# Kernel tuning notes

Hardware: AMD Instinct MI355X
Metric: run time of the kernel (lower is better)

The kernel has to match this reference:

```python
import jax, jax.numpy as jnp
import numpy as np

V = 50257   # vocab size (output_size / num_words)
H = 500     # hidden_size
S = 256     # source sequence length
MAXLEN = 64 # greedy decode steps
SOS = 1


def _gru_scan(xs, Wih, Whh, bih, bhh, reverse=False):
    """Run a GRU over xs: (S, Din) -> (outputs (S,H), final hidden (H,)).
    PyTorch gate order: r, z, n."""
    gx = xs @ Wih.T + bih  # (S, 3H), input-side gates precomputed
    Hh = Whh.shape[1]
    h0 = jnp.zeros((Hh,), dtype=xs.dtype)

    def step(h, g):
        gh = Whh @ h + bhh
        rx, zx, nx = jnp.split(g, 3)
        rh, zh, nh = jnp.split(gh, 3)
        r = jax.nn.sigmoid(rx + rh)
        z = jax.nn.sigmoid(zx + zh)
        n = jnp.tanh(nx + r * nh)
        h2 = (1.0 - z) * n + z * h
        return h2, h2

    hT, ys = jax.lax.scan(step, h0, gx, reverse=reverse)
    return ys, hT


def _gru_cell(x, h, Wih, Whh, bih, bhh):
    gx = Wih @ x + bih
    gh = Whh @ h + bhh
    rx, zx, nx = jnp.split(gx, 3)
    rh, zh, nh = jnp.split(gh, 3)
    r = jax.nn.sigmoid(rx + rh)
    z = jax.nn.sigmoid(zx + zh)
    n = jnp.tanh(nx + r * nh)
    return (1.0 - z) * n + z * h


def setup_inputs() -> dict:
    key = jax.random.key(0)
    ks = jax.random.split(key, 32)

    def p(k, shape):
        return jax.random.normal(k, shape, dtype=jnp.float32) * 0.05

    inp = {}
    inp["input_seq"] = jax.random.randint(ks[0], (S, 1), 0, V)
    inp["input_length"] = S
    inp["max_length"] = MAXLEN
    inp["emb"] = p(ks[1], (V, H))
    i = 2
    for name, din in [("enc0f", H), ("enc0b", H), ("enc1f", 2 * H), ("enc1b", 2 * H)]:
        inp[name + "_Wih"] = p(ks[i], (3 * H, din)); i += 1
        inp[name + "_Whh"] = p(ks[i], (3 * H, H)); i += 1
        inp[name + "_bih"] = p(ks[i], (3 * H,)); i += 1
        inp[name + "_bhh"] = p(ks[i], (3 * H,)); i += 1
    inp["dec_Wih"] = p(ks[i], (2, 3 * H, H)); i += 1
    inp["dec_Whh"] = p(ks[i], (2, 3 * H, H)); i += 1
    inp["dec_bih"] = p(ks[i], (2, 3 * H)); i += 1
    inp["dec_bhh"] = p(ks[i], (2, 3 * H)); i += 1
    inp["concat_W"] = p(ks[i], (H, 2 * H)); i += 1
    inp["concat_b"] = p(ks[i], (H,)); i += 1
    inp["out_W"] = p(ks[i], (V, H)); i += 1
    inp["out_b"] = p(ks[i], (V,)); i += 1
    return inp


def reference(input_seq, input_length, max_length, emb,
              enc0f_Wih, enc0f_Whh, enc0f_bih, enc0f_bhh,
              enc0b_Wih, enc0b_Whh, enc0b_bih, enc0b_bhh,
              enc1f_Wih, enc1f_Whh, enc1f_bih, enc1f_bhh,
              enc1b_Wih, enc1b_Whh, enc1b_bih, enc1b_bhh,
              dec_Wih, dec_Whh, dec_bih, dec_bhh,
              concat_W, concat_b, out_W, out_b):
    tokens = input_seq[:, 0]  # batch = 1
    ex = emb[tokens]          # (S, H) embedding lookup (dropout is eval no-op)

    # --- bidirectional 2-layer encoder GRU (full-length seq, batch=1) ---
    y0f, h0f = _gru_scan(ex, enc0f_Wih, enc0f_Whh, enc0f_bih, enc0f_bhh)
    y0b, h0b = _gru_scan(ex, enc0b_Wih, enc0b_Whh, enc0b_bih, enc0b_bhh, reverse=True)
    x1 = jnp.concatenate([y0f, y0b], axis=1)  # (S, 2H)
    y1f, _ = _gru_scan(x1, enc1f_Wih, enc1f_Whh, enc1f_bih, enc1f_bhh)
    y1b, _ = _gru_scan(x1, enc1b_Wih, enc1b_Whh, enc1b_bih, enc1b_bhh, reverse=True)
    enc_out = y1f + y1b  # (S, H): outputs[:, :H] + outputs[:, H:]

    # encoder_hidden[:n_layers] = [layer0_fwd, layer0_bwd] (PyTorch ordering)
    h_dec0 = jnp.stack([h0f, h0b])  # (2, H)

    def step(carry, _):
        h, tok = carry
        x = emb[tok]  # (H,)
        hs = []
        for l in range(2):  # 2 decoder GRU layers (dropout off in eval)
            hl = _gru_cell(x, h[l], dec_Wih[l], dec_Whh[l], dec_bih[l], dec_bhh[l])
            hs.append(hl)
            x = hl
        h2 = jnp.stack(hs)
        rnn = x  # (H,) top-layer output
        scores = enc_out @ rnn                 # dot attention: (S,)
        w = jax.nn.softmax(scores)
        ctx = w @ enc_out                      # (H,)
        c = jnp.tanh(concat_W @ jnp.concatenate([rnn, ctx]) + concat_b)
        probs = jax.nn.softmax(out_W @ c + out_b)  # (V,)
        tok2 = jnp.argmax(probs).astype(jnp.int32)
        return (h2, tok2), (tok2, probs)

    init = (h_dec0, jnp.asarray(SOS, dtype=jnp.int32))
    _, (all_tokens, all_probs) = jax.lax.scan(step, init, None, length=int(max_length))
    return all_tokens, all_probs
```

## Files before the change

### kernel.cpp

```cpp
#include <hip/hip_runtime.h>
#include <math.h>

typedef unsigned long long ull;

constexpr int H    = 500;
constexpr int H3   = 1500;
constexpr int SEQ  = 256;
constexpr int V    = 50257;
constexpr int TDEC = 64;
constexpr int NLT  = (V + 255) / 256;
constexpr int SB   = 50;
constexpr int UPB  = 10;
constexpr int NDB  = 256;
constexpr int VPB  = (V + NDB - 1) / NDB;

__device__ __forceinline__ float sigmoidf_(float x) { return 1.f / (1.f + expf(-x)); }

__device__ __forceinline__ float wred(float v) {
  #pragma unroll
  for (int off = 32; off > 0; off >>= 1) v += __shfl_down(v, off, 64);
  return v;
}

__device__ __forceinline__ float gload(const float* p) {
  return __hip_atomic_load((float*)p, __ATOMIC_RELAXED, __HIP_MEMORY_SCOPE_AGENT);
}
__device__ __forceinline__ void gstore(float* p, float v) {
  __hip_atomic_store(p, v, __ATOMIC_RELAXED, __HIP_MEMORY_SCOPE_AGENT);
}
__device__ __forceinline__ int gload_i(const int* p) {
  return __hip_atomic_load((int*)p, __ATOMIC_RELAXED, __HIP_MEMORY_SCOPE_AGENT);
}
__device__ __forceinline__ ull gload64(const ull* p) {
  return __hip_atomic_load((ull*)p, __ATOMIC_RELAXED, __HIP_MEMORY_SCOPE_AGENT);
}
__device__ __forceinline__ void gstore64(ull* p, ull v) {
  __hip_atomic_store(p, v, __ATOMIC_RELAXED, __HIP_MEMORY_SCOPE_AGENT);
}

template<int N>
__device__ __forceinline__ void poll_tags(const ull* tags, unsigned want,
                                          float* dst, int tid) {
  constexpr int NW = (N + 63) / 64;
  if (tid < 64) {
    ull v[NW];
    bool ok;
    do {
      ok = true;
      #pragma unroll
      for (int j = 0; j < NW; ++j) {
        int k = tid + (j << 6);
        if (k < N) {
          v[j] = gload64(&tags[k]);
          if ((unsigned)(v[j] >> 32) != want) ok = false;
        }
      }
      if (!ok) __builtin_amdgcn_s_sleep(1);
    } while (!ok);
    #pragma unroll
    for (int j = 0; j < NW; ++j) {
      int k = tid + (j << 6);
      if (k < N) dst[k] = __uint_as_float((unsigned)v[j]);
    }
  }
  __syncthreads();
}

__device__ __forceinline__ void poll2_tags(const ull* tA, float* dA,
                                           const ull* tB, float* dB,
                                           unsigned want, int tid) {
  if (tid < 64) {
    ull va[8], vb[4];
    bool ok;
    do {
      ok = true;
      #pragma unroll
      for (int j = 0; j < 8; ++j) {
        int k = tid + (j << 6);
        if (k < 500) {
          va[j] = gload64(&tA[k]);
          if ((unsigned)(va[j] >> 32) != want) ok = false;
        }
      }
      #pragma unroll
      for (int j = 0; j < 4; ++j) {
        int k = tid + (j << 6);
        vb[j] = gload64(&tB[k]);
        if ((unsigned)(vb[j] >> 32) != want) ok = false;
      }
      if (!ok) __builtin_amdgcn_s_sleep(1);
    } while (!ok);
    #pragma unroll
    for (int j = 0; j < 8; ++j) {
      int k = tid + (j << 6);
      if (k < 500) dA[k] = __uint_as_float((unsigned)va[j]);
    }
    #pragma unroll
    for (int j = 0; j < 4; ++j) {
      int k = tid + (j << 6);
      dB[k] = __uint_as_float((unsigned)vb[j]);
    }
  }
  __syncthreads();
}

__global__ void init_k(ull* ttok) {
  if (threadIdx.x == 0) ttok[0] = (1ull << 32) | 1ull;
}

__global__ void embed_k(const int* __restrict__ seq, const float* __restrict__ emb,
                        float* __restrict__ ex) {
  int t = blockIdx.x;
  int tok = seq[t];
  for (int i = threadIdx.x; i < H; i += blockDim.x)
    ex[(size_t)t * H + i] = emb[(size_t)tok * H + i];
}

__global__ __launch_bounds__(256) void gemm_nt(const float* __restrict__ X,
                                               const float* __restrict__ W,
                                               const float* __restrict__ bias,
                                               float* __restrict__ C,
                                               int M, int N, int K) {
  __shared__ float Xs[64][17];
  __shared__ float Ws[64][17];
  int bm = blockIdx.y * 64, bn = blockIdx.x * 64;
  int tid = threadIdx.x;
  int tx = tid % 16, ty = tid / 16;
  float acc[4][4] = {};
  for (int k0 = 0; k0 < K; k0 += 16) {
    for (int i = tid; i < 64 * 16; i += 256) {
      int m = i / 16, k = i % 16;
      int gm = bm + m, gk = k0 + k, gn = bn + m;
      Xs[m][k] = (gm < M && gk < K) ? X[(size_t)gm * K + gk] : 0.f;
      Ws[m][k] = (gn < N && gk < K) ? W[(size_t)gn * K + gk] : 0.f;
    }
    __syncthreads();
    #pragma unroll
    for (int k = 0; k < 16; ++k) {
      float xv[4], wv[4];
      #pragma unroll
      for (int i = 0; i < 4; ++i) xv[i] = Xs[ty * 4 + i][k];
      #pragma unroll
      for (int j = 0; j < 4; ++j) wv[j] = Ws[tx * 4 + j][k];
      #pragma unroll
      for (int i = 0; i < 4; ++i)
        #pragma unroll
        for (int j = 0; j < 4; ++j) acc[i][j] += xv[i] * wv[j];
    }
    __syncthreads();
  }
  for (int i = 0; i < 4; ++i) {
    int gm = bm + ty * 4 + i;
    if (gm >= M) continue;
    for (int j = 0; j < 4; ++j) {
      int gn = bn + tx * 4 + j;
      if (gn >= N) continue;
      C[(size_t)gm * N + gn] = acc[i][j] + bias[gn];
    }
  }
}

__global__ __launch_bounds__(512, 1) void gru_scan_tag(
    const float* __restrict__ gxF, const float* __restrict__ gxB,
    const float* __restrict__ WhhF, const float* __restrict__ WhhB,
    const float* __restrict__ bhhF, const float* __restrict__ bhhB,
    ull* __restrict__ tAF, ull* __restrict__ tBF,
    ull* __restrict__ tAB, ull* __restrict__ tBB,
    float* __restrict__ yF, float* __restrict__ yB, int ystride) {
  __shared__ float gates[32];
  __shared__ float h_lds[512];
  int dir = blockIdx.x / SB;
  int bu  = blockIdx.x % SB;
  int u0  = bu * UPB;
  const float* gx  = dir ? gxB : gxF;
  const float* Whh = dir ? WhhB : WhhF;
  const float* bhh = dir ? bhhB : bhhF;
  ull* tagA = dir ? tAB : tAF;
  ull* tagB = dir ? tBB : tBF;
  float* y  = dir ? yB : yF;
  int tid = threadIdx.x, lane = tid & 63, wid = tid >> 6;

  float wreg[4][8];
  #pragma unroll
  for (int rr = 0; rr < 4; ++rr) {
    int r = wid + 8 * rr;
    #pragma unroll
    for (int j = 0; j < 8; ++j) {
      int k = lane + 64 * j;
      wreg[rr][j] = (r < 30 && k < 500)
          ? Whh[(size_t)((r / UPB) * 500 + u0 + (r % UPB)) * 500 + k] : 0.f;
    }
  }
  int u = u0 + tid;
  float br = 0.f, bz = 0.f, bn = 0.f;
  if (tid < UPB) { br = bhh[u]; bz = bhh[500 + u]; bn = bhh[1000 + u]; }
  h_lds[tid] = 0.f;
  __syncthreads();

  for (int t = 0; t < SEQ; ++t) {
    ull* wout = (t & 1) ? tagA : tagB;
    ull* win  = (t & 1) ? tagB : tagA;
    int teff = dir ? (SEQ - 1 - t) : t;

    float gxr = 0.f, gxz = 0.f, gxn = 0.f;
    if (tid < UPB) {
      const float* g = gx + (size_t)teff * H3;
      gxr = g[u]; gxz = g[500 + u]; gxn = g[1000 + u];
    }

    if (t > 0 && wid == 0) {
      ull v[8];
      for (;;) {
        bool ok = true;
        #pragma unroll
        for (int j = 0; j < 8; ++j) {
          int k = lane + 64 * j;
          if (k < 500) {
            v[j] = gload64(&win[k]);
            if ((unsigned)(v[j] >> 32) != (unsigned)t) ok = false;
          }
        }
        if (ok) break;
        __builtin_amdgcn_s_sleep(1);
      }
      #pragma unroll
      for (int j = 0; j < 8; ++j) {
        int k = lane + 64 * j;
        if (k < 500) h_lds[k] = __uint_as_float((unsigned)v[j]);
      }
    }
    __syncthreads();

    float hreg[8];
    #pragma unroll
    for (int j = 0; j < 8; ++j) {
      int k = lane + 64 * j;
      hreg[j] = (k < 500) ? h_lds[k] : 0.f;
    }
    #pragma unroll
    for (int rr = 0; rr < 4; ++rr) {
      int r = wid + 8 * rr;
      if (r < 30) {
        float acc = 0.f;
        #pragma unroll
        for (int j = 0; j < 8; ++j) acc += wreg[rr][j] * hreg[j];
        acc = wred(acc);
        if (lane == 0) gates[r] = acc;
      }
    }
    __syncthreads();
    if (tid < UPB) {
      float hold = h_lds[u];
      float rr = sigmoidf_(gxr + gates[tid]           + br);
      float zz = sigmoidf_(gxz + gates[UPB + tid]     + bz);
      float nn = tanhf(    gxn + rr * (gates[2 * UPB + tid] + bn));
      float hp = (1.f - zz) * nn + zz * hold;
      ull pv = ((ull)(unsigned)(t + 1) << 32) | (ull)__float_as_uint(hp);
      gstore64(&wout[u], pv);
      y[(size_t)teff * ystride + u] = hp;
    }
    __syncthreads();
  }
}

__global__ void seed_k(const ull* __restrict__ tf, const ull* __restrict__ tb,
                       ull* __restrict__ th0a, ull* __restrict__ th1a) {
  int i = threadIdx.x;
  if (i < 500) {
    th0a[i] = (ull)(unsigned)tf[i];
    th1a[i] = (ull)(unsigned)tb[i];
  }
}

__global__ void add_k(const float* __restrict__ a, const float* __restrict__ b,
                      float* __restrict__ c, int n) {
  int i = blockIdx.x * blockDim.x + threadIdx.x;
  if (i < n) c[i] = a[i] + b[i];
}

__device__ __forceinline__ void cell_unit_tag(int u, int lane,
    const float* xf, const float* hf,
    const float* __restrict__ Wih, const float* __restrict__ Whh,
    const float* __restrict__ bih, const float* __restrict__ bhh,
    ull* htag, unsigned want) {
  float g[6];
  #pragma unroll
  for (int kind = 0; kind < 6; ++kind) {
    const float* row = (kind < 3) ? (Wih + (size_t)(kind * 500 + u) * 500)
                                  : (Whh + (size_t)((kind - 3) * 500 + u) * 500);
    const float* vec = (kind < 3) ? xf : hf;
    float acc = 0.f;
    #pragma unroll
    for (int j = 0; j < 8; ++j) {
      int k = lane + 64 * j;
      if (k < 500) acc += row[k] * vec[k];
    }
    g[kind] = wred(acc);
  }
  if (lane == 0) {
    float r = sigmoidf_(g[0] + bih[u]        + g[3] + bhh[u]);
    float z = sigmoidf_(g[1] + bih[500 + u]  + g[4] + bhh[500 + u]);
    float n = tanhf(    g[2] + bih[1000 + u] + r * (g[5] + bhh[1000 + u]));
    float hv = (1.f - z) * n + z * hf[u];
    gstore64(&htag[u], ((ull)want << 32) | (ull)__float_as_uint(hv));
  }
}

__global__ __launch_bounds__(512, 1) void dec_persist(
    const float* __restrict__ emb,
    const float* __restrict__ dWih, const float* __restrict__ dWhh,
    const float* __restrict__ dbih, const float* __restrict__ dbhh,
    const float* __restrict__ enc_out, const float* __restrict__ cW,
    const float* __restrict__ cb,
    const float* __restrict__ outW, const float* __restrict__ outb,
    ull* __restrict__ th0a, ull* __restrict__ th0b,
    ull* __restrict__ th1a, ull* __restrict__ th1b,
    ull* __restrict__ tsc, ull* __restrict__ tctx, ull* __restrict__ tcvec,
    ull* __restrict__ ttok,
    float* __restrict__ lg0, float* __restrict__ lg1,
    float* __restrict__ pm, float* __restrict__ ps, int* __restrict__ pix,
    float* __restrict__ stats, float* __restrict__ out_tokens,
    float* __restrict__ out_probs, int* __restrict__ dcnt) {
  __shared__ float4 v4[250];
  __shared__ float hfull[512];
  __shared__ float red[256], sc[256];
  __shared__ float wm[8], wsum[8]; __shared__ int wix[8];
  __shared__ float mm[256], ms[256]; __shared__ int mi[256];
  __shared__ int lastf, sh_tk;
  float* xf = (float*)v4;
  float* hf = xf + 500;
  int tid = threadIdx.x, lane = tid & 63, wid = tid >> 6, blk = blockIdx.x;
  bool worker = blk < 63;
  int u = blk * 8 + wid;

  for (int st = 0; st < TDEC; ++st) {
    unsigned want = (unsigned)(st + 1);
    ull* h0r = (st & 1) ? th0b : th0a;
    ull* h0w = (st & 1) ? th0a : th0b;
    ull* h1r = (st & 1) ? th1b : th1a;
    ull* h1w = (st & 1) ? th1a : th1b;
    float* lg_w = (st & 1) ? lg1 : lg0;
    const float* lg_r = (st & 1) ? lg0 : lg1;

    if (worker) {
      if (tid == 0) {
        ull tv;
        for (;;) {
          tv = gload64(ttok);
          if ((unsigned)(tv >> 32) == want) break;
          __builtin_amdgcn_s_sleep(1);
        }
        sh_tk = (int)(unsigned)tv;
      }
      __syncthreads();
      int tk = sh_tk;
      if (tid >= 64) {
        for (int i = tid - 64; i < 500; i += 448) xf[i] = emb[(size_t)tk * 500 + i];
      } else {
        #pragma unroll
        for (int j = 0; j < 8; ++j) {
          int k = tid + (j << 6);
          if (k < 500) hf[k] = __uint_as_float((unsigned)gload64(&h0r[k]));
        }
      }
      __syncthreads();
      if (u < 500) cell_unit_tag(u, lane, xf, hf, dWih, dWhh, dbih, dbhh, h0w, want);
      __syncthreads();

      if (tid >= 64) {
        for (int i = tid - 64; i < 500; i += 448)
          hf[i] = __uint_as_float((unsigned)gload64(&h1r[i]));
      }
      poll_tags<500>(h0w, want, xf, tid);
      if (u < 500) cell_unit_tag(u, lane, xf, hf,
          dWih + 750000, dWhh + 750000, dbih + 1500, dbhh + 1500, h1w, want);
      __syncthreads();

      if (blk < 32) {
        poll_tags<500>(h1w, want, hfull, tid);
        int s = blk * 8 + wid;
        const float* row = enc_out + (size_t)s * 500;
        float acc = 0.f;
        #pragma unroll
        for (int j = 0; j < 8; ++j) {
          int k = lane + 64 * j;
          if (k < 500) acc += row[k] * hfull[k];
        }
        acc = wred(acc);
        if (lane == 0) gstore64(&tsc[s], ((ull)want << 32) | (ull)__float_as_uint(acc));
        poll_tags<256>(tsc, want, sc, tid);
      } else {
        poll2_tags(h1w, hfull, tsc, sc, want, tid);
      }

      {
        float myv = (tid < 256) ? sc[tid] : 0.f;
        if (tid < 256) red[tid] = myv;
        __syncthreads();
        for (int s = 128; s > 0; s >>= 1) {
          if (tid < s) red[tid] = fmaxf(red[tid], red[tid + s]);
          __syncthreads();
        }
        float m = red[0]; __syncthreads();
        float e = 0.f;
        if (tid < 256) { e = expf(myv - m); red[tid] = e; }
        __syncthreads();
        for (int s = 128; s > 0; s >>= 1) {
          if (tid < s) red[tid] += red[tid + s];
          __syncthreads();
        }
        float inv = 1.f / red[0]; __syncthreads();
        if (tid < 256) sc[tid] = e * inv;
        __syncthreads();
        int j = blk * 8 + wid;
        if (j < 500) {
          float acc = 0.f;
          #pragma unroll
          for (int q = 0; q < 4; ++q) {
            int s = lane + 64 * q;
            acc += sc[s] * enc_out[(size_t)s * 500 + j];
          }
          acc = wred(acc);
          if (lane == 0) gstore64(&tctx[j], ((ull)want << 32) | (ull)__float_as_uint(acc));
        }
      }

      if (tid >= 64) for (int i = tid - 64; i < 500; i += 448) xf[i] = hfull[i];
      poll_tags<500>(tctx, want, hf, tid);
      {
        int i = blk * 8 + wid;
        if (i < 500) {
          const float* row = cW + (size_t)i * 1000;
          float acc = 0.f;
          #pragma unroll
          for (int j = 0; j < 16; ++j) {
            int k = lane + 64 * j;
            if (k < 1000) acc += row[k] * xf[k];
          }
          acc = wred(acc);
          if (lane == 0)
            gstore64(&tcvec[i], ((ull)want << 32) | (ull)__float_as_uint(tanhf(acc + cb[i])));
        }
      }
      __syncthreads();
    }

    poll_tags<500>(tcvec, want, xf, tid);
    const float4* c4 = v4;
    {
      int lstart = wid * 25, lend = (wid + 1) * 25; if (lend > VPB) lend = VPB;
      int r0 = blk * VPB + lstart, r1 = blk * VPB + lend; if (r1 > V) r1 = V;
      float m = -1e30f, ssum = 0.f; int ix = V;
      for (int rb = r0; rb < r1; rb += 4) {
        int nr = r1 - rb; if (nr > 4) nr = 4;
        float a[4] = {0.f, 0.f, 0.f, 0.f};
        #pragma unroll
        for (int q = 0; q < 2; ++q) {
          int k4 = lane + 64 * q;
          if (k4 < 125) {
            float4 cc = c4[k4];
            #pragma unroll
            for (int rr = 0; rr < 4; ++rr) {
              if (rr < nr) {
                float4 w4 = ((const float4*)(outW + (size_t)(rb + rr) * 500))[k4];
                a[rr] += w4.x * cc.x + w4.y * cc.y + w4.z * cc.z + w4.w * cc.w;
              }
            }
          }
        }
        #pragma unroll
        for (int rr = 0; rr < 4; ++rr) {
          if (rr < nr) {
            float l = wred(a[rr]);
            if (lane == 0) {
              l += outb[rb + rr];
              lg_w[rb + rr] = l;
              if (l > m) { ssum = ssum * expf(m - l) + 1.f; m = l; ix = rb + rr; }
              else       { ssum += expf(l - m); }
            }
          }
        }
      }
      if (lane == 0) { wm[wid] = m; wsum[wid] = ssum; wix[wid] = ix; }
    }
    __syncthreads();
    if (tid == 0) {
      float M = wm[0], S = wsum[0]; int I = wix[0];
      for (int w2 = 1; w2 < 8; ++w2) {
        if (wm[w2] > M) { S = S * expf(M - wm[w2]) + wsum[w2]; M = wm[w2]; I = wix[w2]; }
        else            { S += wsum[w2] * expf(wm[w2] - M); }
      }
      gstore(&pm[blk], M); gstore(&ps[blk], S);
      __hip_atomic_store(&pix[blk], I, __ATOMIC_RELAXED, __HIP_MEMORY_SCOPE_AGENT);
      __builtin_amdgcn_s_waitcnt(0);
      int prev = __hip_atomic_fetch_add(&dcnt[st], 1, __ATOMIC_RELAXED,
                                        __HIP_MEMORY_SCOPE_AGENT);
      lastf = (prev == NDB - 1) ? 1 : 0;
    }
    __syncthreads();

    if (lastf) {
      if (tid < 256) { mm[tid] = gload(&pm[tid]); ms[tid] = gload(&ps[tid]); mi[tid] = gload_i(&pix[tid]); }
      __syncthreads();
      for (int s = 128; s > 0; s >>= 1) {
        if (tid < s) {
          float ma = mm[tid], mb = mm[tid + s];
          float sa = ms[tid], sb = ms[tid + s];
          int ia = mi[tid], ib = mi[tid + s];
          if (mb > ma || (mb == ma && ib < ia)) {
            ms[tid] = sa * expf(ma - mb) + sb; mm[tid] = mb; mi[tid] = ib;
          } else {
            ms[tid] = sa + sb * expf(mb - ma);
          }
        }
        __syncthreads();
      }
      if (tid == 0) {
        out_tokens[st] = (float)mi[0];
        gstore(&stats[2 * st], mm[0]);
        gstore(&stats[2 * st + 1], 1.f / ms[0]);
        __builtin_amdgcn_s_waitcnt(0);
        gstore64(ttok, ((ull)(unsigned)(st + 2) << 32) | (ull)(unsigned)mi[0]);
      }
    }

    if (st > 0) {
      float mM = gload(&stats[2 * (st - 1)]), iS = gload(&stats[2 * (st - 1) + 1]);
      int base = blk * VPB;
      for (int r = tid; r < VPB; r += 512) {
        int v = base + r;
        if (v < V) out_probs[(size_t)(st - 1) * V + v] = expf(lg_r[v] - mM) * iS;
      }
    }
    __syncthreads();
  }
}

__global__ __launch_bounds__(256) void probs_k(const float* __restrict__ logits,
    const float* __restrict__ stats, float* __restrict__ out_probs) {
  int v = blockIdx.x * 256 + threadIdx.x;
  if (v < V) out_probs[v] = expf(logits[v] - stats[0]) * stats[1];
}

extern "C" void kernel_launch(void* const* d_in, const int* in_sizes, int n_in,
                              void* d_out, int out_size, void* d_ws, size_t ws_size,
                              hipStream_t stream) {
  const int*   seq   = (const int*)d_in[0];
  const float* emb   = (const float*)d_in[3];
  const float* e0f_Wih = (const float*)d_in[4];
  const float* e0f_Whh = (const float*)d_in[5];
  const float* e0f_bih = (const float*)d_in[6];
  const float* e0f_bhh = (const float*)d_in[7];
  const float* e0b_Wih = (const float*)d_in[8];
  const float* e0b_Whh = (const float*)d_in[9];
  const float* e0b_bih = (const float*)d_in[10];
  const float* e0b_bhh = (const float*)d_in[11];
  const float* e1f_Wih = (const float*)d_in[12];
  const float* e1f_Whh = (const float*)d_in[13];
  const float* e1f_bih = (const float*)d_in[14];
  const float* e1f_bhh = (const float*)d_in[15];
  const float* e1b_Wih = (const float*)d_in[16];
  const float* e1b_Whh = (const float*)d_in[17];
  const float* e1b_bih = (const float*)d_in[18];
  const float* e1b_bhh = (const float*)d_in[19];
  const float* dWih = (const float*)d_in[20];
  const float* dWhh = (const float*)d_in[21];
  const float* dbih = (const float*)d_in[22];
  const float* dbhh = (const float*)d_in[23];
  const float* cW   = (const float*)d_in[24];
  const float* cb   = (const float*)d_in[25];
  const float* outW = (const float*)d_in[26];
  const float* outb = (const float*)d_in[27];

  float* w = (float*)d_ws;
  float* ex      = w;
  float* x1      = ex + 128000;
  float* gxf     = x1 + 256000;
  float* gxb     = gxf + 384000;
  float* y1f     = gxb + 384000;
  float* y1b     = y1f + 128000;
  float* enc_out = y1b + 128000;
  float* lg0     = enc_out + 128000;
  float* lg1     = lg0 + 50432;
  float* pm      = lg1 + 50432;
  float* ps      = pm + 256;
  float* stats   = ps + 256;
  int*   pix     = (int*)(stats + 192);
  int*   dcnt    = pix + 256;
  ull*   htag    = (ull*)(dcnt + 64);
  ull* tL0F_A = htag;        ull* tL0F_B = htag + 512;
  ull* tL0B_A = htag + 1024; ull* tL0B_B = htag + 1536;
  ull* tL1F_A = htag + 2048; ull* tL1F_B = htag + 2560;
  ull* tL1B_A = htag + 3072; ull* tL1B_B = htag + 3584;
  ull*   dtag    = htag + 4096;
  ull* th0a  = dtag;        ull* th0b = dtag + 512;
  ull* th1a  = dtag + 1024; ull* th1b = dtag + 1536;
  ull* tsc   = dtag + 2048; ull* tctx = dtag + 2304;
  ull* tcvec = dtag + 2816; ull* ttok = dtag + 3328;

  float* outf = (float*)d_out;

  hipMemsetAsync(dcnt, 0, 64 * sizeof(int) + 7488 * sizeof(ull), stream);

  init_k<<<1, 64, 0, stream>>>(ttok);
  embed_k<<<SEQ, 128, 0, stream>>>(seq, emb, ex);

  gemm_nt<<<dim3(24, 4), 256, 0, stream>>>(ex, e0f_Wih, e0f_bih, gxf, SEQ, H3, H);
  gemm_nt<<<dim3(24, 4), 256, 0, stream>>>(ex, e0b_Wih, e0b_bih, gxb, SEQ, H3, H);
  gru_scan_tag<<<2 * SB, 512, 0, stream>>>(gxf, gxb, e0f_Whh, e0b_Whh,
      e0f_bhh, e0b_bhh, tL0F_A, tL0F_B, tL0B_A, tL0B_B, x1, x1 + 500, 1000);

  gemm_nt<<<dim3(24, 4), 256, 0, stream>>>(x1, e1f_Wih, e1f_bih, gxf, SEQ, H3, 2 * H);
  gemm_nt<<<dim3(24, 4), 256, 0, stream>>>(x1, e1b_Wih, e1b_bih, gxb, SEQ, H3, 2 * H);
  gru_scan_tag<<<2 * SB, 512, 0, stream>>>(gxf, gxb, e1f_Whh, e1b_Whh,
      e1f_bhh, e1b_bhh, tL1F_A, tL1F_B, tL1B_A, tL1B_B, y1f, y1b, 500);
  add_k<<<(SEQ * H + 255) / 256, 256, 0, stream>>>(y1f, y1b, enc_out, SEQ * H);

  seed_k<<<1, 512, 0, stream>>>(tL0F_A, tL0B_A, th0a, th1a);

  dec_persist<<<NDB, 512, 0, stream>>>(emb,
      dWih, dWhh, dbih, dbhh, enc_out, cW, cb, outW, outb,
      th0a, th0b, th1a, th1b, tsc, tctx, tcvec, ttok,
      lg0, lg1, pm, ps, pix, stats, outf, outf + TDEC, dcnt);

  probs_k<<<NLT, 256, 0, stream>>>(((TDEC - 1) & 1) ? lg1 : lg0,
      stats + 2 * (TDEC - 1), outf + TDEC + (size_t)(TDEC - 1) * V);
}
```

Before: 6.212 ms.

## Restructure decoder into 32 wide worker blocks with transposed encoder outputs

The persistent decoder now launches 1024-thread blocks and concentrates the recurrent, attention and concat work in 32 worker blocks of 16 waves each, down from 63 blocks of 8 waves. The remaining blocks wait on the token tag and write out the previous step's probabilities while the workers compute. A transposed copy of enc_out is built so the context reduction reads contiguous columns. The vocab projection now handles 8 rows per pass, and a redundant syncthreads was removed from the encoder scan. Larger blocks raise register pressure, and the workers take on more serial work per step.

After: 6.665 ms. +7.3%, slower.

```diff
diff --git a/kernel.cpp b/kernel.cpp
--- a/kernel.cpp
+++ b/kernel.cpp
@@ -13,6 +13,7 @@
 constexpr int UPB  = 10;
 constexpr int NDB  = 256;
 constexpr int VPB  = (V + NDB - 1) / NDB;
+constexpr int WB   = 32;
 
 __device__ __forceinline__ float sigmoidf_(float x) { return 1.f / (1.f + expf(-x)); }
 
@@ -38,7 +39,7 @@
   __hip_atomic_store(p, v, __ATOMIC_RELAXED, __HIP_MEMORY_SCOPE_AGENT);
 }
 
-template<int N>
+template<int N, int SLP>
 __device__ __forceinline__ void poll_tags(const ull* tags, unsigned want,
                                           float* dst, int tid) {
   constexpr int NW = (N + 63) / 64;
@@ -55,50 +56,12 @@
           if ((unsigned)(v[j] >> 32) != want) ok = false;
         }
       }
-      if (!ok) __builtin_amdgcn_s_sleep(1);
+      if (!ok) __builtin_amdgcn_s_sleep(SLP);
     } while (!ok);
     #pragma unroll
     for (int j = 0; j < NW; ++j) {
       int k = tid + (j << 6);
       if (k < N) dst[k] = __uint_as_float((unsigned)v[j]);
-    }
-  }
-  __syncthreads();
-}
-
-__device__ __forceinline__ void poll2_tags(const ull* tA, float* dA,
-                                           const ull* tB, float* dB,
-                                           unsigned want, int tid) {
-  if (tid < 64) {
-    ull va[8], vb[4];
-    bool ok;
-    do {
-      ok = true;
-      #pragma unroll
-      for (int j = 0; j < 8; ++j) {
-        int k = tid + (j << 6);
-        if (k < 500) {
-          va[j] = gload64(&tA[k]);
-          if ((unsigned)(va[j] >> 32) != want) ok = false;
-        }
-      }
-      #pragma unroll
-      for (int j = 0; j < 4; ++j) {
-        int k = tid + (j << 6);
-        vb[j] = gload64(&tB[k]);
-        if ((unsigned)(vb[j] >> 32) != want) ok = false;
-      }
-      if (!ok) __builtin_amdgcn_s_sleep(1);
-    } while (!ok);
-    #pragma unroll
-    for (int j = 0; j < 8; ++j) {
-      int k = tid + (j << 6);
-      if (k < 500) dA[k] = __uint_as_float((unsigned)va[j]);
-    }
-    #pragma unroll
-    for (int j = 0; j < 4; ++j) {
-      int k = tid + (j << 6);
-      dB[k] = __uint_as_float((unsigned)vb[j]);
     }
   }
   __syncthreads();
@@ -231,6 +194,7 @@
     }
     __syncthreads();
 
+    float hold = (tid < UPB) ? h_lds[u] : 0.f;
     float hreg[8];
     #pragma unroll
     for (int j = 0; j < 8; ++j) {
@@ -250,7 +214,6 @@
     }
     __syncthreads();
     if (tid < UPB) {
-      float hold = h_lds[u];
       float rr = sigmoidf_(gxr + gates[tid]           + br);
       float zz = sigmoidf_(gxz + gates[UPB + tid]     + bz);
       float nn = tanhf(    gxn + rr * (gates[2 * UPB + tid] + bn));
@@ -259,7 +222,6 @@
       gstore64(&wout[u], pv);
       y[(size_t)teff * ystride + u] = hp;
     }
-    __syncthreads();
   }
 }
 
@@ -276,6 +238,25 @@
                       float* __restrict__ c, int n) {
   int i = blockIdx.x * blockDim.x + threadIdx.x;
   if (i < n) c[i] = a[i] + b[i];
+}
+
+__global__ __launch_bounds__(256) void transposeE_k(const float* __restrict__ A,
+                                                    float* __restrict__ B) {
+  __shared__ float t[64][65];
+  int c0 = blockIdx.x * 64;
+  int r0 = blockIdx.y * 64;
+  int tx = threadIdx.x & 63, ty = threadIdx.x >> 6;
+  #pragma unroll
+  for (int i = 0; i < 64; i += 4) {
+    int r = r0 + ty + i, c = c0 + tx;
+    if (r < SEQ && c < 500) t[ty + i][tx] = A[(size_t)r * 500 + c];
+  }
+  __syncthreads();
+  #pragma unroll
+  for (int i = 0; i < 64; i += 4) {
+    int c = c0 + ty + i, r = r0 + tx;
+    if (c < 500 && r < SEQ) B[(size_t)c * SEQ + r] = t[tx][ty + i];
+  }
 }
 
 __device__ __forceinline__ void cell_unit_tag(int u, int lane,
@@ -306,12 +287,12 @@
   }
 }
 
-__global__ __launch_bounds__(512, 1) void dec_persist(
+__global__ __launch_bounds__(1024, 4) void dec_persist(
     const float* __restrict__ emb,
     const float* __restrict__ dWih, const float* __restrict__ dWhh,
     const float* __restrict__ dbih, const float* __restrict__ dbhh,
-    const float* __restrict__ enc_out, const float* __restrict__ cW,
-    const float* __restrict__ cb,
+    const float* __restrict__ enc_out, const float* __restrict__ enc_outT,
+    const float* __restrict__ cW, const float* __restrict__ cb,
     const float* __restrict__ outW, const float* __restrict__ outb,
     ull* __restrict__ th0a, ull* __restrict__ th0b,
     ull* __restrict__ th1a, ull* __restrict__ th1b,
@@ -324,14 +305,14 @@
   __shared__ float4 v4[250];
   __shared__ float hfull[512];
   __shared__ float red[256], sc[256];
-  __shared__ float wm[8], wsum[8]; __shared__ int wix[8];
+  __shared__ float wm[16], wsum[16]; __shared__ int wix[16];
   __shared__ float mm[256], ms[256]; __shared__ int mi[256];
   __shared__ int lastf, sh_tk;
   float* xf = (float*)v4;
   float* hf = xf + 500;
   int tid = threadIdx.x, lane = tid & 63, wid = tid >> 6, blk = blockIdx.x;
-  bool worker = blk < 63;
-  int u = blk * 8 + wid;
+  bool worker = blk < WB;
+  int u = blk * 16 + wid;
 
   for (int st = 0; st < TDEC; ++st) {
     unsigned want = (unsigned)(st + 1);
@@ -355,7 +336,7 @@
       __syncthreads();
       int tk = sh_tk;
       if (tid >= 64) {
-        for (int i = tid - 64; i < 500; i += 448) xf[i] = emb[(size_t)tk * 500 + i];
+        for (int i = tid - 64; i < 500; i += 960) xf[i] = emb[(size_t)tk * 500 + i];
       } else {
         #pragma unroll
         for (int j = 0; j < 8; ++j) {
@@ -368,16 +349,15 @@
       __syncthreads();
 
       if (tid >= 64) {
-        for (int i = tid - 64; i < 500; i += 448)
+        for (int i = tid - 64; i < 500; i += 960)
           hf[i] = __uint_as_float((unsigned)gload64(&h1r[i]));
       }
-      poll_tags<500>(h0w, want, xf, tid);
+      poll_tags<500, 1>(h0w, want, xf, tid);
       if (u < 500) cell_unit_tag(u, lane, xf, hf,
           dWih + 750000, dWhh + 750000, dbih + 1500, dbhh + 1500, h1w, want);
-      __syncthreads();
-
-      if (blk < 32) {
-        poll_tags<500>(h1w, want, hfull, tid);
+
+      poll_tags<500, 1>(h1w, want, hfull, tid);
+      if (wid < 8) {
         int s = blk * 8 + wid;
         const float* row = enc_out + (size_t)s * 500;
         float acc = 0.f;
@@ -388,10 +368,8 @@
         }
         acc = wred(acc);
         if (lane == 0) gstore64(&tsc[s], ((ull)want << 32) | (ull)__float_as_uint(acc));
-        poll_tags<256>(tsc, want, sc, tid);
-      } else {
-        poll2_tags(h1w, hfull, tsc, sc, want, tid);
-      }
+      }
+      poll_tags<256, 1>(tsc, want, sc, tid);
 
       {
         float myv = (tid < 256) ? sc[tid] : 0.f;
@@ -412,23 +390,24 @@
         float inv = 1.f / red[0]; __syncthreads();
         if (tid < 256) sc[tid] = e * inv;
         __syncthreads();
-        int j = blk * 8 + wid;
+        int j = blk * 16 + wid;
         if (j < 500) {
+          const float* col = enc_outT + (size_t)j * SEQ;
           float acc = 0.f;
           #pragma unroll
           for (int q = 0; q < 4; ++q) {
             int s = lane + 64 * q;
-            acc += sc[s] * enc_out[(size_t)s * 500 + j];
+            acc += sc[s] * col[s];
           }
           acc = wred(acc);
           if (lane == 0) gstore64(&tctx[j], ((ull)want << 32) | (ull)__float_as_uint(acc));
         }
       }
 
-      if (tid >= 64) for (int i = tid - 64; i < 500; i += 448) xf[i] = hfull[i];
-      poll_tags<500>(tctx, want, hf, tid);
+      if (tid >= 64) for (int i = tid - 64; i < 500; i += 960) xf[i] = hfull[i];
+      poll_tags<500, 1>(tctx, want, hf, tid);
       {
-        int i = blk * 8 + wid;
+        int i = blk * 16 + wid;
         if (i < 500) {
           const float* row = cW + (size_t)i * 1000;
           float acc = 0.f;
@@ -443,24 +422,40 @@
         }
       }
       __syncthreads();
-    }
-
-    poll_tags<500>(tcvec, want, xf, tid);
+    } else {
+      if (tid == 0) {
+        while ((unsigned)(gload64(ttok) >> 32) < want) __builtin_amdgcn_s_sleep(2);
+      }
+      __syncthreads();
+      if (st > 0) {
+        float mM = gload(&stats[2 * (st - 1)]), iS = gload(&stats[2 * (st - 1) + 1]);
+        int base = blk * VPB;
+        for (int r = tid; r < VPB; r += 1024) {
+          int v = base + r;
+          if (v < V) out_probs[(size_t)(st - 1) * V + v] = expf(lg_r[v] - mM) * iS;
+        }
+      }
+    }
+
+    if (worker) poll_tags<500, 1>(tcvec, want, xf, tid);
+    else        poll_tags<500, 4>(tcvec, want, xf, tid);
     const float4* c4 = v4;
     {
-      int lstart = wid * 25, lend = (wid + 1) * 25; if (lend > VPB) lend = VPB;
+      int lstart = wid * 13, lend = lstart + 13;
+      if (lstart > VPB) lstart = VPB;
+      if (lend > VPB) lend = VPB;
       int r0 = blk * VPB + lstart, r1 = blk * VPB + lend; if (r1 > V) r1 = V;
       float m = -1e30f, ssum = 0.f; int ix = V;
-      for (int rb = r0; rb < r1; rb += 4) {
-        int nr = r1 - rb; if (nr > 4) nr = 4;
-        float a[4] = {0.f, 0.f, 0.f, 0.f};
+      for (int rb = r0; rb < r1; rb += 8) {
+        int nr = r1 - rb; if (nr > 8) nr = 8;
+        float a[8] = {0.f, 0.f, 0.f, 0.f, 0.f, 0.f, 0.f, 0.f};
         #pragma unroll
         for (int q = 0; q < 2; ++q) {
           int k4 = lane + 64 * q;
           if (k4 < 125) {
             float4 cc = c4[k4];
             #pragma unroll
-            for (int rr = 0; rr < 4; ++rr) {
+            for (int rr = 0; rr < 8; ++rr) {
               if (rr < nr) {
                 float4 w4 = ((const float4*)(outW + (size_t)(rb + rr) * 500))[k4];
                 a[rr] += w4.x * cc.x + w4.y * cc.y + w4.z * cc.z + w4.w * cc.w;
@@ -469,7 +464,7 @@
           }
         }
         #pragma unroll
-        for (int rr = 0; rr < 4; ++rr) {
+        for (int rr = 0; rr < 8; ++rr) {
           if (rr < nr) {
             float l = wred(a[rr]);
             if (lane == 0) {
@@ -486,7 +481,7 @@
     __syncthreads();
     if (tid == 0) {
       float M = wm[0], S = wsum[0]; int I = wix[0];
-      for (int w2 = 1; w2 < 8; ++w2) {
+      for (int w2 = 1; w2 < 16; ++w2) {
         if (wm[w2] > M) { S = S * expf(M - wm[w2]) + wsum[w2]; M = wm[w2]; I = wix[w2]; }
         else            { S += wsum[w2] * expf(wm[w2] - M); }
       }
@@ -524,10 +519,10 @@
       }
     }
 
-    if (st > 0) {
+    if (worker && st > 0) {
       float mM = gload(&stats[2 * (st - 1)]), iS = gload(&stats[2 * (st - 1) + 1]);
       int base = blk * VPB;
-      for (int r = tid; r < VPB; r += 512) {
+      for (int r = tid; r < VPB; r += 1024) {
         int v = base + r;
         if (v < V) out_probs[(size_t)(st - 1) * V + v] = expf(lg_r[v] - mM) * iS;
       }
@@ -597,10 +592,11 @@
   ull* th1a  = dtag + 1024; ull* th1b = dtag + 1536;
   ull* tsc   = dtag + 2048; ull* tctx = dtag + 2304;
   ull* tcvec = dtag + 2816; ull* ttok = dtag + 3328;
+  float* enc_outT = (float*)(dtag + 3400);
 
   float* outf = (float*)d_out;
 
-  hipMemsetAsync(dcnt, 0, 64 * sizeof(int) + 7488 * sizeof(ull), stream);
+  (void)hipMemsetAsync(dcnt, 0, 64 * sizeof(int) + 7488 * sizeof(ull), stream);
 
   init_k<<<1, 64, 0, stream>>>(ttok);
   embed_k<<<SEQ, 128, 0, stream>>>(seq, emb, ex);
@@ -615,11 +611,12 @@
   gru_scan_tag<<<2 * SB, 512, 0, stream>>>(gxf, gxb, e1f_Whh, e1b_Whh,
       e1f_bhh, e1b_bhh, tL1F_A, tL1F_B, tL1B_A, tL1B_B, y1f, y1b, 500);
   add_k<<<(SEQ * H + 255) / 256, 256, 0, stream>>>(y1f, y1b, enc_out, SEQ * H);
+  transposeE_k<<<dim3(8, 4), 256, 0, stream>>>(enc_out, enc_outT);
 
   seed_k<<<1, 512, 0, stream>>>(tL0F_A, tL0B_A, th0a, th1a);
 
-  dec_persist<<<NDB, 512, 0, stream>>>(emb,
-      dWih, dWhh, dbih, dbhh, enc_out, cW, cb, outW, outb,
+  dec_persist<<<NDB, 1024, 0, stream>>>(emb,
+      dWih, dWhh, dbih, dbhh, enc_out, enc_outT, cW, cb, outW, outb,
       th0a, th0b, th1a, th1b, tsc, tctx, tcvec, ttok,
       lg0, lg1, pm, ps, pix, stats, outf, outf + TDEC, dcnt);
 
```
